# Optimization experiments

Hardware: AMD Instinct MI355X
Metric: run time of the kernel (lower is better)

## Reference

```python
import jax, jax.numpy as jnp
import numpy as np

B, S, D = 32, 128, 1024      # encoder batch, seq len, embed_dim
C = 65536                    # nclasses (sense inventory)
N = 512                      # number of gathered WSD target tokens
NNZ = 262144                 # nnz of sparse label adjacency A (avg degree 4)
EPS = 1e-5                   # BatchNorm1d eps


def setup_inputs() -> dict:
    key = jax.random.key(0)
    ks = jax.random.split(key, 7)
    enc_out = jax.random.normal(ks[0], (B, S, D), dtype=jnp.float32)
    batch_idx = jax.random.randint(ks[1], (N,), 0, B)
    tgt = jax.random.randint(ks[2], (N,), 0, S)
    A_indices = jax.random.randint(ks[3], (2, NNZ), 0, C)
    A_values = jax.random.uniform(ks[4], (NNZ,), dtype=jnp.float32)
    wt2_w = jax.random.normal(ks[5], (C, D), dtype=jnp.float32) / np.sqrt(D).astype(np.float32)
    wt2_b = jax.random.normal(ks[6], (C,), dtype=jnp.float32) * 0.02
    return {"enc_out": enc_out, "wt2_w": wt2_w, "wt2_b": wt2_b,
            "A_values": A_values, "batch_idx": batch_idx, "tgt": tgt,
            "A_indices": A_indices}


def reference(enc_out, wt2_w, wt2_b, A_values, batch_idx, tgt, A_indices):
    # gather target-token embeddings: [N, D]
    g = enc_out[batch_idx, tgt]
    # BatchNorm1d(affine=False), training mode -> batch stats, biased var
    mean = jnp.mean(g, axis=0)
    var = jnp.var(g, axis=0)
    h0 = (g - mean) / jnp.sqrt(var + EPS)
    # wt2 Linear + swish -> logits over classes Z: [N, C]
    h1 = jax.nn.swish(h0 @ wt2_w.T + wt2_b)
    # sparse spmm: torch_sparse.spmm(ii, vv, m=C, n=C, matrix=Z.T).T == Z @ A.T
    row, col = A_indices[0], A_indices[1]
    gathered = h1.T[col] * A_values[:, None]            # [NNZ, N]
    neighbors = jax.ops.segment_sum(gathered, row, num_segments=C).T  # [N, C]
    # residual add (renormalize=False)
    return neighbors + h1
```

## Files before the change

kernel.cpp:

```cpp
#include <hip/hip_runtime.h>
#include <hip/hip_bf16.h>

typedef unsigned short u16;
typedef unsigned int   u32;
typedef __attribute__((ext_vector_type(8))) short bf16x8;
typedef __attribute__((ext_vector_type(4))) float f32x4;

static constexpr int kS = 128, kD = 1024, kC = 65536, kN = 512, kNNZ = 262144;

__device__ __forceinline__ u16 f2bf(float x) {
  u32 u = __float_as_uint(x);
  u32 r = (u + 0x7fffu + ((u >> 16) & 1u)) >> 16;
  return (u16)r;
}
__device__ __forceinline__ u32 pack2(float a, float b) {
  return (u32)f2bf(a) | ((u32)f2bf(b) << 16);
}
__device__ __forceinline__ float bf_lo(u32 v) { return __uint_as_float(v << 16); }
__device__ __forceinline__ float bf_hi(u32 v) { return __uint_as_float(v & 0xffff0000u); }

__device__ __forceinline__ void gload16(const void* g, void* l) {
  __builtin_amdgcn_global_load_lds(
      (const __attribute__((address_space(1))) void*)g,
      (__attribute__((address_space(3))) void*)l, 16, 0, 0);
}

__global__ void k_bn_part(const float* __restrict__ enc, const int* __restrict__ bidx,
                          const int* __restrict__ tgt, float* __restrict__ part) {
  __shared__ int offs[64];
  int n0 = blockIdx.y * 64;
  if (threadIdx.x < 64) offs[threadIdx.x] = bidx[n0 + threadIdx.x] * kS + tgt[n0 + threadIdx.x];
  __syncthreads();
  int d = blockIdx.x * 256 + threadIdx.x;
  float s = 0.f, ss = 0.f;
  for (int i = 0; i < 64; ++i) {
    float v = enc[(size_t)offs[i] * kD + d];
    s += v; ss += v * v;
  }
  part[(blockIdx.y * 2 + 0) * kD + d] = s;
  part[(blockIdx.y * 2 + 1) * kD + d] = ss;
}

__global__ void k_bn_fin(const float* __restrict__ part, float* __restrict__ mean,
                         float* __restrict__ rstd) {
  int d = blockIdx.x * 256 + threadIdx.x;
  float s = 0.f, ss = 0.f;
#pragma unroll
  for (int b = 0; b < 8; ++b) {
    s  += part[(b * 2 + 0) * kD + d];
    ss += part[(b * 2 + 1) * kD + d];
  }
  float m = s * (1.f / kN);
  float var = ss * (1.f / kN) - m * m;
  mean[d] = m;
  rstd[d] = 1.f / sqrtf(var + 1e-5f);
}

__global__ void k_bn_pack(const float* __restrict__ enc, const int* __restrict__ bidx,
                          const int* __restrict__ tgt, const float* __restrict__ mean,
                          const float* __restrict__ rstd, u16* __restrict__ Bp) {
  int i = blockIdx.x * 256 + threadIdx.x;
  int n = i & 511;
  int g = i >> 9;
  int k0 = g * 8;
  size_t src = (size_t)(bidx[n] * kS + tgt[n]) * kD + k0;
  float4 v0 = *(const float4*)(enc + src);
  float4 v1 = *(const float4*)(enc + src + 4);
  float4 m0 = *(const float4*)(mean + k0);
  float4 m1 = *(const float4*)(mean + k0 + 4);
  float4 r0 = *(const float4*)(rstd + k0);
  float4 r1 = *(const float4*)(rstd + k0 + 4);
  u32 q0 = pack2((v0.x - m0.x) * r0.x, (v0.y - m0.y) * r0.y);
  u32 q1 = pack2((v0.z - m0.z) * r0.z, (v0.w - m0.w) * r0.w);
  u32 q2 = pack2((v1.x - m1.x) * r1.x, (v1.y - m1.y) * r1.y);
  u32 q3 = pack2((v1.z - m1.z) * r1.z, (v1.w - m1.w) * r1.w);
  *(uint4*)(Bp + (size_t)i * 8) = make_uint4(q0, q1, q2, q3);
}

__global__ void k_hist(const int* __restrict__ rows, int* __restrict__ hist) {
  int e = blockIdx.x * blockDim.x + threadIdx.x;
  if (e < kNNZ) atomicAdd(&hist[rows[e]], 1);
}

__global__ __launch_bounds__(1024) void k_scan(int* __restrict__ hist, int* __restrict__ cursor) {
  __shared__ int sm[1024];
  int t = threadIdx.x;
  int base = t * 64;
  int sum = 0;
  for (int i = 0; i < 64; ++i) sum += hist[base + i];
  sm[t] = sum;
  __syncthreads();
  for (int off = 1; off < 1024; off <<= 1) {
    int v = (t >= off) ? sm[t - off] : 0;
    __syncthreads();
    sm[t] += v;
    __syncthreads();
  }
  int run = sm[t] - sum;
  for (int i = 0; i < 64; ++i) {
    int v = hist[base + i];
    hist[base + i] = run;
    cursor[base + i] = run;
    run += v;
  }
  if (t == 1023) hist[kC] = run;
}

__global__ void k_scatter(const int* __restrict__ rows, const int* __restrict__ cols,
                          const float* __restrict__ vals, int* __restrict__ cursor,
                          int* __restrict__ scol, float* __restrict__ sval) {
  int e = blockIdx.x * blockDim.x + threadIdx.x;
  if (e < kNNZ) {
    int r = rows[e];
    int p = atomicAdd(&cursor[r], 1);
    scol[p] = cols[e];
    sval[p] = vals[e];
  }
}

__global__ __launch_bounds__(512, 4)
void k_gemm_f4(const float* __restrict__ W, const u16* __restrict__ Bp,
               const float* __restrict__ bias, u16* __restrict__ h1t) {
  __shared__ __align__(16) float Ab0[64 * 64];
  __shared__ __align__(16) float Ab1[64 * 64];
  const int t = threadIdx.x;
  const int l = t & 63;
  const int w = t >> 6;
  const int wn = w * 64;
  const int cb = blockIdx.x * 64;
  const int q = l >> 4, ln = l & 15;

  const int s0 = t, s1 = t + 512;
  const int r0s = s0 >> 4, c0 = (s0 & 15) ^ (r0s & 7);
  const int r1s = s1 >> 4, c1 = (s1 & 15) ^ (r1s & 7);
  const float* g0 = W + (size_t)(cb + r0s) * kD + c0 * 4;
  const float* g1 = W + (size_t)(cb + r1s) * kD + c1 * 4;

  const u16* gB = Bp + (size_t)q * 4096 + (size_t)(wn + ln) * 8;

  f32x4 acc[4][4];
#pragma unroll
  for (int a = 0; a < 4; ++a)
#pragma unroll
    for (int b = 0; b < 4; ++b) acc[a][b] = (f32x4){0.f, 0.f, 0.f, 0.f};

  gload16(g0, (char*)Ab0 + s0 * 16);
  gload16(g1, (char*)Ab1 - 16384 + s1 * 16);
  __syncthreads();

#pragma unroll 1
  for (int tt = 0; tt < 16; ++tt) {
    const float* cur = (tt & 1) ? Ab1 : Ab0;
    float* nxt = (tt & 1) ? Ab0 : Ab1;
    if (tt < 15) {
      size_t go = (size_t)(tt + 1) * 64;
      gload16(g0 + go, (char*)nxt + s0 * 16);
      gload16(g1 + go, (char*)nxt + s1 * 16);
    }
#pragma unroll
    for (int ks = 0; ks < 2; ++ks) {
      bf16x8 bv[4];
#pragma unroll
      for (int nb = 0; nb < 4; ++nb)
        bv[nb] = *(const bf16x8*)(gB + (size_t)(tt * 8 + ks * 4) * 4096 + nb * 128);
#pragma unroll
      for (int mb = 0; mb < 4; ++mb) {
        int rr = mb * 16 + ln;
        int sb = ks * 8 + q * 2;
        const char* rowp = (const char*)cur + rr * 256;
        float4 a0 = *(const float4*)(rowp + ((sb + 0) ^ (rr & 7)) * 16);
        float4 a1 = *(const float4*)(rowp + ((sb + 1) ^ (rr & 7)) * 16);
        union { u32 u[4]; bf16x8 v; } cvt;
        cvt.u[0] = pack2(a0.x, a0.y);
        cvt.u[1] = pack2(a0.z, a0.w);
        cvt.u[2] = pack2(a1.x, a1.y);
        cvt.u[3] = pack2(a1.z, a1.w);
#pragma unroll
        for (int nb = 0; nb < 4; ++nb)
          acc[mb][nb] = __builtin_amdgcn_mfma_f32_16x16x32_bf16(cvt.v, bv[nb], acc[mb][nb], 0, 0, 0);
      }
    }
    __syncthreads();
  }

#pragma unroll
  for (int mb = 0; mb < 4; ++mb) {
    int rb = mb * 16 + q * 4;
#pragma unroll
    for (int i = 0; i < 4; ++i) {
      int c = cb + rb + i;
      float bvs = bias[c];
#pragma unroll
      for (int nb = 0; nb < 4; ++nb) {
        float x = acc[mb][nb][i] + bvs;
        float sw = x / (1.f + __expf(-x));
        h1t[(size_t)c * kN + (wn + nb * 16 + ln)] = f2bf(sw);
      }
    }
  }
}

#define FMA8(cv, v)                                                        \
  a0 = fmaf(v, bf_lo(cv.x), a0); a1 = fmaf(v, bf_hi(cv.x), a1);            \
  a2 = fmaf(v, bf_lo(cv.y), a2); a3 = fmaf(v, bf_hi(cv.y), a3);            \
  a4 = fmaf(v, bf_lo(cv.z), a4); a5 = fmaf(v, bf_hi(cv.z), a5);            \
  a6 = fmaf(v, bf_lo(cv.w), a6); a7 = fmaf(v, bf_hi(cv.w), a7);

__global__ __launch_bounds__(512)
void k_spmm(const u16* __restrict__ h1t, const int* __restrict__ rowptr,
            const int* __restrict__ scol, const float* __restrict__ sval,
            float* __restrict__ out) {
  __shared__ float tile[32 * 512];
  int r0 = blockIdx.x * 32;
  int t = threadIdx.x, w = t >> 6, l = t & 63;
#pragma unroll
  for (int j = 0; j < 4; ++j) {
    int rl = w * 4 + j;
    int r = r0 + rl;
    uint4 hv = ((const uint4*)(h1t + (size_t)r * kN))[l];
    float a0 = bf_lo(hv.x), a1 = bf_hi(hv.x), a2 = bf_lo(hv.y), a3 = bf_hi(hv.y);
    float a4 = bf_lo(hv.z), a5 = bf_hi(hv.z), a6 = bf_lo(hv.w), a7 = bf_hi(hv.w);
    int e0 = rowptr[r], e1 = rowptr[r + 1];
    uint4 cv0 = {}, cv1 = {};
    float v0 = 0.f, v1 = 0.f;
    if (e0 < e1) {
      v0 = sval[e0];
      cv0 = ((const uint4*)(h1t + (size_t)scol[e0] * kN))[l];
    }
    if (e0 + 1 < e1) {
      v1 = sval[e0 + 1];
      cv1 = ((const uint4*)(h1t + (size_t)scol[e0 + 1] * kN))[l];
    }
    for (int e = e0; e < e1; e += 2) {
      FMA8(cv0, v0);
      if (e + 2 < e1) {
        v0 = sval[e + 2];
        cv0 = ((const uint4*)(h1t + (size_t)scol[e + 2] * kN))[l];
      }
      if (e + 1 < e1) {
        FMA8(cv1, v1);
        if (e + 3 < e1) {
          v1 = sval[e + 3];
          cv1 = ((const uint4*)(h1t + (size_t)scol[e + 3] * kN))[l];
        }
      }
    }
    int sw = (rl & 7) << 2;
    *(float4*)&tile[rl * 512 + ((8 * l) ^ sw)]     = make_float4(a0, a1, a2, a3);
    *(float4*)&tile[rl * 512 + ((8 * l + 4) ^ sw)] = make_float4(a4, a5, a6, a7);
  }
  __syncthreads();
  int r = l & 31;
  int swr = (r & 7) << 2;
#pragma unroll
  for (int it = 0; it < 32; ++it) {
    int n = it * 16 + w * 2 + (l >> 5);
    out[(size_t)n * kC + r0 + r] = tile[r * 512 + (n ^ swr)];
  }
}

extern "C" void kernel_launch(void* const* d_in, const int* in_sizes, int n_in,
                              void* d_out, int out_size, void* d_ws, size_t ws_size,
                              hipStream_t stream) {
  (void)in_sizes; (void)n_in; (void)out_size; (void)ws_size;
  const float* enc   = (const float*)d_in[0];
  const float* W     = (const float*)d_in[1];
  const float* bias  = (const float*)d_in[2];
  const float* Avals = (const float*)d_in[3];
  const int*   bidx  = (const int*)d_in[4];
  const int*   tgt   = (const int*)d_in[5];
  const int*   Arow  = (const int*)d_in[6];
  const int*   Acol  = Arow + kNNZ;
  float* out = (float*)d_out;

  char* ws = (char*)d_ws;
  float* mean   = (float*)(ws);
  float* rstd   = (float*)(ws + 4096);
  u16*   Bp     = (u16*)  (ws + 8192);
  int*   rowptr = (int*)  (ws + 1056768);
  int*   cursor = (int*)  (ws + 1319168);
  int*   scol   = (int*)  (ws + 1581312);
  float* sval   = (float*)(ws + 2629888);
  float* part   = (float*)(ws + 3678464);
  u16*   h1t    = (u16*)  (ws + 4194304);

  hipMemsetAsync(rowptr, 0, (kC + 1) * sizeof(int), stream);
  k_bn_part<<<dim3(4, 8), 256, 0, stream>>>(enc, bidx, tgt, part);
  k_bn_fin<<<4, 256, 0, stream>>>(part, mean, rstd);
  k_bn_pack<<<256, 256, 0, stream>>>(enc, bidx, tgt, mean, rstd, Bp);
  k_hist<<<kNNZ / 256, 256, 0, stream>>>(Arow, rowptr);
  k_scan<<<1, 1024, 0, stream>>>(rowptr, cursor);
  k_scatter<<<kNNZ / 256, 256, 0, stream>>>(Arow, Acol, Avals, cursor, scol, sval);
  k_gemm_f4<<<kC / 64, 512, 0, stream>>>(W, Bp, bias, h1t);
  k_spmm<<<kC / 32, 512, 0, stream>>>(h1t, rowptr, scol, sval, out);
}
```

Baseline: 299.3 us.

## Convert W tile to bf16 once in registers before storing to LDS

Replaces the direct global-to-LDS fp32 loads of the weight tile with register loads that are converted to bf16 once by each staging thread and then written to a swizzled bf16 LDS buffer. The previous version had every wave convert fp32 to bf16 after reading from LDS, so each element was converted several times and LDS traffic and footprint were doubled. The new version halves LDS usage and removes the redundant conversions. In exchange it gives up the asynchronous LDS-direct loads, so register pressure and exposed load latency may rise. It also switches to the library round-to-nearest conversion and unrolls the main loop by 2.

```diff
diff --git a/kernel.cpp b/kernel.cpp
--- a/kernel.cpp
+++ b/kernel.cpp
@@ -16,14 +16,13 @@
 __device__ __forceinline__ u32 pack2(float a, float b) {
   return (u32)f2bf(a) | ((u32)f2bf(b) << 16);
 }
+__device__ __forceinline__ u32 pk(float a, float b) {
+  __hip_bfloat162 h = __float22bfloat162_rn(float2{a, b});
+  union { __hip_bfloat162 v; u32 u; } c; c.v = h;
+  return c.u;
+}
 __device__ __forceinline__ float bf_lo(u32 v) { return __uint_as_float(v << 16); }
 __device__ __forceinline__ float bf_hi(u32 v) { return __uint_as_float(v & 0xffff0000u); }
-
-__device__ __forceinline__ void gload16(const void* g, void* l) {
-  __builtin_amdgcn_global_load_lds(
-      (const __attribute__((address_space(1))) void*)g,
-      (__attribute__((address_space(3))) void*)l, 16, 0, 0);
-}
 
 __global__ void k_bn_part(const float* __restrict__ enc, const int* __restrict__ bidx,
                           const int* __restrict__ tgt, float* __restrict__ part) {
@@ -119,22 +118,18 @@
 }
 
 __global__ __launch_bounds__(512, 4)
-void k_gemm_f4(const float* __restrict__ W, const u16* __restrict__ Bp,
+void k_gemm_f5(const float* __restrict__ W, const u16* __restrict__ Bp,
                const float* __restrict__ bias, u16* __restrict__ h1t) {
-  __shared__ __align__(16) float Ab0[64 * 64];
-  __shared__ __align__(16) float Ab1[64 * 64];
+  __shared__ __align__(16) u16 Ab[2 * 64 * 64];
   const int t = threadIdx.x;
-  const int l = t & 63;
-  const int w = t >> 6;
+  const int l = t & 63, w = t >> 6;
   const int wn = w * 64;
   const int cb = blockIdx.x * 64;
   const int q = l >> 4, ln = l & 15;
 
-  const int s0 = t, s1 = t + 512;
-  const int r0s = s0 >> 4, c0 = (s0 & 15) ^ (r0s & 7);
-  const int r1s = s1 >> 4, c1 = (s1 & 15) ^ (r1s & 7);
-  const float* g0 = W + (size_t)(cb + r0s) * kD + c0 * 4;
-  const float* g1 = W + (size_t)(cb + r1s) * kD + c1 * 4;
+  const int sr = t >> 3, sc = t & 7;
+  const float* gA = W + (size_t)(cb + sr) * kD + sc * 8;
+  const int swoff = sr * 64 + ((sc ^ (sr & 7)) * 8);
 
   const u16* gB = Bp + (size_t)q * 4096 + (size_t)(wn + ln) * 8;
 
@@ -144,41 +139,41 @@
 #pragma unroll
     for (int b = 0; b < 4; ++b) acc[a][b] = (f32x4){0.f, 0.f, 0.f, 0.f};
 
-  gload16(g0, (char*)Ab0 + s0 * 16);
-  gload16(g1, (char*)Ab1 - 16384 + s1 * 16);
-  __syncthreads();
-
-#pragma unroll 1
+  {
+    float4 a0 = *(const float4*)(gA);
+    float4 a1 = *(const float4*)(gA + 4);
+    *(uint4*)(Ab + swoff) =
+        make_uint4(pk(a0.x, a0.y), pk(a0.z, a0.w), pk(a1.x, a1.y), pk(a1.z, a1.w));
+  }
+  __syncthreads();
+
+#pragma unroll 2
   for (int tt = 0; tt < 16; ++tt) {
-    const float* cur = (tt & 1) ? Ab1 : Ab0;
-    float* nxt = (tt & 1) ? Ab0 : Ab1;
+    const int cur = tt & 1;
+    float4 na0, na1;
     if (tt < 15) {
-      size_t go = (size_t)(tt + 1) * 64;
-      gload16(g0 + go, (char*)nxt + s0 * 16);
-      gload16(g1 + go, (char*)nxt + s1 * 16);
-    }
+      na0 = *(const float4*)(gA + (tt + 1) * 64);
+      na1 = *(const float4*)(gA + (tt + 1) * 64 + 4);
+    }
+    const u16* curb = Ab + cur * 4096;
 #pragma unroll
     for (int ks = 0; ks < 2; ++ks) {
       bf16x8 bv[4];
 #pragma unroll
       for (int nb = 0; nb < 4; ++nb)
-        bv[nb] = *(const bf16x8*)(gB + (size_t)(tt * 8 + ks * 4) * 4096 + nb * 128);
+        bv[nb] = *(const bf16x8*)(gB + (size_t)((tt * 8 + ks * 4) * 4096) + nb * 128);
 #pragma unroll
       for (int mb = 0; mb < 4; ++mb) {
         int rr = mb * 16 + ln;
-        int sb = ks * 8 + q * 2;
-        const char* rowp = (const char*)cur + rr * 256;
-        float4 a0 = *(const float4*)(rowp + ((sb + 0) ^ (rr & 7)) * 16);
-        float4 a1 = *(const float4*)(rowp + ((sb + 1) ^ (rr & 7)) * 16);
-        union { u32 u[4]; bf16x8 v; } cvt;
-        cvt.u[0] = pack2(a0.x, a0.y);
-        cvt.u[1] = pack2(a0.z, a0.w);
-        cvt.u[2] = pack2(a1.x, a1.y);
-        cvt.u[3] = pack2(a1.z, a1.w);
+        bf16x8 af = *(const bf16x8*)(curb + rr * 64 + (((ks * 4 + q) ^ (rr & 7)) * 8));
 #pragma unroll
         for (int nb = 0; nb < 4; ++nb)
-          acc[mb][nb] = __builtin_amdgcn_mfma_f32_16x16x32_bf16(cvt.v, bv[nb], acc[mb][nb], 0, 0, 0);
-      }
+          acc[mb][nb] = __builtin_amdgcn_mfma_f32_16x16x32_bf16(af, bv[nb], acc[mb][nb], 0, 0, 0);
+      }
+    }
+    if (tt < 15) {
+      *(uint4*)(Ab + (cur ^ 1) * 4096 + swoff) =
+          make_uint4(pk(na0.x, na0.y), pk(na0.z, na0.w), pk(na1.x, na1.y), pk(na1.z, na1.w));
     }
     __syncthreads();
   }
@@ -291,6 +286,6 @@
   k_hist<<<kNNZ / 256, 256, 0, stream>>>(Arow, rowptr);
   k_scan<<<1, 1024, 0, stream>>>(rowptr, cursor);
   k_scatter<<<kNNZ / 256, 256, 0, stream>>>(Arow, Acol, Avals, cursor, scol, sval);
-  k_gemm_f4<<<kC / 64, 512, 0, stream>>>(W, Bp, bias, h1t);
+  k_gemm_f5<<<kC / 64, 512, 0, stream>>>(W, Bp, bias, h1t);
   k_spmm<<<kC / 32, 512, 0, stream>>>(h1t, rowptr, scol, sval, out);
 }
```

Result: no change. 294.4 us (-1.6%).
